# Kernel optimization log

Measured on AMD Instinct MI355X. Metric: run time of the kernel, lower is better.

## Reference

```python
import jax, jax.numpy as jnp
import numpy as np

ALPHA = 0.01  # alpha = input_scale * weight_scale (dequant scale)
BETA = 1.0    # bias scale, fixed to 1.0 in forward


def setup_inputs() -> dict:
    key = jax.random.key(0)
    k1, k2, k3 = jax.random.split(key, 3)
    # int8 values carried in int32 containers (schema has no int8 dtype)
    x = jax.random.randint(k1, (2, 2048, 4096), -127, 128, dtype=jnp.int32)
    weight = jax.random.randint(k2, (11008, 4096), -127, 128, dtype=jnp.int32)
    bias = jax.random.normal(k3, (1, 11008), dtype=jnp.float32)
    return {"x": x, "weight": weight, "bias": bias}


def reference(x, weight, bias):
    # x: [..., K] int8 activations, weight: [N, K] int8, bias: [1, N] fp32
    x_shape = x.shape
    x2 = x.reshape(-1, x_shape[-1]).astype(jnp.int8)   # [M, K]
    w8 = weight.astype(jnp.int8)                        # [N, K]
    acc = jnp.einsum('mk,nk->mn', x2, w8, preferred_element_type=jnp.int32)
    # fused dequant scale + fp32 bias add
    y = ALPHA * acc.astype(jnp.float32) + BETA * bias   # [M, N]
    return y.reshape(*x_shape[:-1], -1)
```

## Files before the change

kernel.cpp:

```cpp
#include <hip/hip_runtime.h>


#define M_DIM 4096
#define N_DIM 11008
#define K_DIM 4096
#define BM 256
#define BN 256
#define BK 128
#define NT (K_DIM / BK)
#define ALPHA 0.01f

typedef __attribute__((ext_vector_type(4))) int i32x4;

static __device__ __forceinline__ int pack4(int4 v) {
    return (v.x & 0xff) | ((v.y & 0xff) << 8) |
           ((v.z & 0xff) << 16) | ((unsigned)(v.w & 0xff) << 24);
}

__global__ __launch_bounds__(256) void pack_i8_kernel(
    const int4* __restrict__ x, int4* __restrict__ xout, int n16x,
    const int4* __restrict__ w, int4* __restrict__ wout, int n16_total)
{
    int i = blockIdx.x * blockDim.x + threadIdx.x;
    if (i >= n16_total) return;
    const int4* src;
    int4* dst;
    int idx;
    if (i < n16x) { src = x; dst = xout; idx = i; }
    else          { src = w; dst = wout; idx = i - n16x; }
    const int4* p = src + (size_t)4 * idx;
    int4 a = p[0], b = p[1], c = p[2], d = p[3];
    int4 r;
    r.x = pack4(a); r.y = pack4(b); r.z = pack4(c); r.w = pack4(d);
    dst[idx] = r;
}

#define GA0 (s_ + 8 * (s_ >> 3))
#define GA1 (8 + s_ + 8 * (s_ >> 3))
#define GB0 ((s_ & 3) + 8 * (s_ >> 2))
#define GB1 (4 + (s_ & 3) + 8 * (s_ >> 2))

#define STAGE(dstArr, srcB, T, GEXPR)                                          \
    _Pragma("unroll") for (int u_ = 0; u_ < 2; u_++) {                         \
        const int s_ = u_ * 8 + wave;                                          \
        const int G_ = (GEXPR);                                                \
        __builtin_amdgcn_global_load_lds(                                      \
            (const __attribute__((address_space(1))) void*)(                   \
                (srcB) + (size_t)(G_ * 8 + (lane >> 3)) * K_DIM +              \
                (size_t)(T) * BK + sch16),                                     \
            (__attribute__((address_space(3))) void*)((dstArr) + G_ * 1024 +   \
                                                      lane * 16),              \
            16, 0, 0);                                                         \
    }

#define READ_A(Arr, dst, IB)                                                   \
    _Pragma("unroll") for (int i_ = 0; i_ < 4; i_++)                           \
        _Pragma("unroll") for (int k_ = 0; k_ < 2; k_++)                       \
            dst[i_][k_] = *(const i32x4*)((Arr) + aoff[k_] + ((IB) + i_) * 2048);

#define READ_B(Arr, dst, JB)                                                   \
    _Pragma("unroll") for (int j_ = 0; j_ < 2; j_++)                           \
        _Pragma("unroll") for (int k_ = 0; k_ < 2; k_++)                       \
            dst[j_][k_] = *(const i32x4*)((Arr) + boff[k_] + ((JB) + j_) * 2048);

#define MFMA_G(af, bf, IB, JB)                                                 \
    __builtin_amdgcn_s_setprio(1);                                             \
    _Pragma("unroll") for (int i_ = 0; i_ < 4; i_++)                           \
        _Pragma("unroll") for (int j_ = 0; j_ < 2; j_++)                       \
            _Pragma("unroll") for (int k_ = 0; k_ < 2; k_++)                   \
                acc[(IB) + i_][(JB) + j_] =                                    \
                    __builtin_amdgcn_mfma_i32_16x16x64_i8(                     \
                        af[i_][k_], bf[j_][k_],                                \
                        acc[(IB) + i_][(JB) + j_], 0, 0, 0);                   \
    __builtin_amdgcn_s_setprio(0);

#define VMCNT_(N) asm volatile("s_waitcnt vmcnt(" #N ")" ::: "memory")
#define VMCNT(N) VMCNT_(N)
#define BAR() __builtin_amdgcn_s_barrier()

#define TILE(CA, CB, NA, NB, T, STG, V1, V2, V3, V4)                           \
    {                                                                          \
              \
        READ_A(CA, ra0, 0);                                                    \
        if (STG) { STAGE(NA, Abase, (T) + 1, GA0); }                           \
        VMCNT(V1);                                                             \
        BAR();                                                                 \
        READ_B(CB, rb01, 0);                                                   \
        MFMA_G(ra0, rb01, 0, 0);                                               \
        BAR();                                                                 \
                         \
        if (STG) { STAGE(NB, Bbase, (T) + 1, GB0); }                           \
        VMCNT(V2);                                                             \
        BAR();                                                                 \
        READ_B(CB, rb23, 2);                                                   \
        MFMA_G(ra0, rb23, 0, 2);                                               \
        BAR();                                                                 \
                          \
        if (STG) { STAGE(NB, Bbase, (T) + 1, GB1); }                           \
        VMCNT(V3);                                                             \
        BAR();                                                                 \
        READ_A(CA, ra1, 4);                                                    \
        MFMA_G(ra1, rb23, 4, 2);                                               \
        BAR();                                                                 \
                      \
        READ_B(CB, rb01, 0);                                                   \
        if (STG) { STAGE(NA, Abase, (T) + 1, GA1); }                           \
        VMCNT(V4);                                                             \
        BAR();                                                                 \
        MFMA_G(ra1, rb01, 4, 0);                                               \
        BAR();                                                                 \
    }

__global__ __launch_bounds__(512, 1) void gemm_i8_kernel(
    const char* __restrict__ A,
    const char* __restrict__ B,
    const float* __restrict__ bias,
    float* __restrict__ C)
{
    __shared__ __attribute__((aligned(16))) char As0[BM * BK];
    __shared__ __attribute__((aligned(16))) char Bs0[BN * BK];
    __shared__ __attribute__((aligned(16))) char As1[BM * BK];
    __shared__ __attribute__((aligned(16))) char Bs1[BN * BK];

    const int tid   = threadIdx.x;
    const int lane  = tid & 63;
    const int wave  = tid >> 6;
    const int waveM = (wave >> 2) * 128;
    const int waveN = (wave & 3) * 64;
    const int lrow  = lane & 15;
    const int lquad = lane >> 4;

    const int bid = blockIdx.x;
    const int xcd = bid & 7;
    const int loc = bid >> 3;
    const int bm  = (2 * xcd + (loc & 1)) * BM;
    const int bn  = (loc >> 1) * BN;

    const int sch16 = ((lane & 7) ^ ((lane >> 3) & 7)) << 4;
    const char* Abase = A + (size_t)bm * K_DIM;
    const char* Bbase = B + (size_t)bn * K_DIM;

    int aoff[2], boff[2];
#pragma unroll
    for (int ks = 0; ks < 2; ks++) {
        const int pos = ((ks * 4 + lquad) ^ (lrow & 7)) << 4;
        aoff[ks] = (waveM + lrow) * BK + pos;
        boff[ks] = (waveN + lrow) * BK + pos;
    }

    i32x4 acc[8][4] = {};
    i32x4 ra0[4][2], ra1[4][2], rb01[2][2], rb23[2][2];

    STAGE(As0, Abase, 0, GA0);
    STAGE(Bs0, Bbase, 0, GB0);
    STAGE(Bs0, Bbase, 0, GB1);
    STAGE(As0, Abase, 0, GA1);
    VMCNT(0);
    BAR();

#pragma unroll 1
    for (int t = 0; t < NT - 2; t += 2) {
        TILE(As0, Bs0, As1, Bs1, t,     1, 6, 6, 6, 6);
        TILE(As1, Bs1, As0, Bs0, t + 1, 1, 6, 6, 6, 6);
    }
    TILE(As0, Bs0, As1, Bs1, NT - 2, 1, 6, 6, 6, 6);
    TILE(As1, Bs1, As0, Bs0, NT - 1, 0, 4, 2, 0, 0);

#pragma unroll
    for (int i = 0; i < 8; i++) {
        const int r0 = bm + waveM + i * 16 + lquad * 4;
#pragma unroll
        for (int j = 0; j < 4; j++) {
            const int c0 = bn + waveN + j * 16 + lrow;
            const float bv = bias[c0];
#pragma unroll
            for (int r = 0; r < 4; r++) {
                C[(size_t)(r0 + r) * N_DIM + c0] = ALPHA * (float)acc[i][j][r] + bv;
            }
        }
    }
}

extern "C" void kernel_launch(void* const* d_in, const int* in_sizes, int n_in,
                              void* d_out, int out_size, void* d_ws, size_t ws_size,
                              hipStream_t stream) {
    const int*   x    = (const int*)d_in[0];
    const int*   w    = (const int*)d_in[1];
    const float* bias = (const float*)d_in[2];
    float*       out  = (float*)d_out;

    char* Ap = (char*)d_ws;
    char* Wp = (char*)d_ws + (size_t)M_DIM * K_DIM;

    const int n16x = M_DIM * K_DIM / 16;
    const int n16w = N_DIM * K_DIM / 16;
    const int n16  = n16x + n16w;
    pack_i8_kernel<<<n16 / 256, 256, 0, stream>>>(
        (const int4*)x, (int4*)Ap, n16x, (const int4*)w, (int4*)Wp, n16);

    gemm_i8_kernel<<<dim3((M_DIM / BM) * (N_DIM / BN)), 512, 0, stream>>>(
        Ap, Wp, bias, out);
}
```

Baseline: 541.6 us.

## Load B fragments directly from global into registers, bypassing LDS

Removes the LDS staging buffers for the weight (B) tile. Each wave now loads its B fragments straight from global memory into registers, one K-tile ahead, and the barrier count per tile drops from eight to two. The aim is to halve LDS traffic and shared-memory footprint and to cut synchronisation. The cost is uncoalesced 16-byte-per-lane global loads for B with no reuse across waves, plus longer VMCNT waits and more register pressure from double-buffered B fragments.

After: 604.8 us. +11.7%, slower.

```diff
diff --git a/kernel.cpp b/kernel.cpp
--- a/kernel.cpp
+++ b/kernel.cpp
@@ -37,8 +37,6 @@
 
 #define GA0 (s_ + 8 * (s_ >> 3))
 #define GA1 (8 + s_ + 8 * (s_ >> 3))
-#define GB0 ((s_ & 3) + 8 * (s_ >> 2))
-#define GB1 (4 + (s_ & 3) + 8 * (s_ >> 2))
 
 #define STAGE(dstArr, srcB, T, GEXPR)                                          \
     _Pragma("unroll") for (int u_ = 0; u_ < 2; u_++) {                         \
@@ -58,16 +56,20 @@
         _Pragma("unroll") for (int k_ = 0; k_ < 2; k_++)                       \
             dst[i_][k_] = *(const i32x4*)((Arr) + aoff[k_] + ((IB) + i_) * 2048);
 
-#define READ_B(Arr, dst, JB)                                                   \
+#define BLOAD01(dst, IMM)                                                      \
     _Pragma("unroll") for (int j_ = 0; j_ < 2; j_++)                           \
         _Pragma("unroll") for (int k_ = 0; k_ < 2; k_++)                       \
-            dst[j_][k_] = *(const i32x4*)((Arr) + boff[k_] + ((JB) + j_) * 2048);
+            dst[j_][k_] = *(const i32x4*)(bptr[j_] + (IMM) + k_ * 64);
+#define BLOAD23(dst, IMM)                                                      \
+    _Pragma("unroll") for (int j_ = 0; j_ < 2; j_++)                           \
+        _Pragma("unroll") for (int k_ = 0; k_ < 2; k_++)                       \
+            dst[j_][k_] = *(const i32x4*)(bptr[2 + j_] + (IMM) + k_ * 64);
 
 #define MFMA_G(af, bf, IB, JB)                                                 \
     __builtin_amdgcn_s_setprio(1);                                             \
-    _Pragma("unroll") for (int i_ = 0; i_ < 4; i_++)                           \
-        _Pragma("unroll") for (int j_ = 0; j_ < 2; j_++)                       \
-            _Pragma("unroll") for (int k_ = 0; k_ < 2; k_++)                   \
+    _Pragma("unroll") for (int k_ = 0; k_ < 2; k_++)                           \
+        _Pragma("unroll") for (int i_ = 0; i_ < 4; i_++)                       \
+            _Pragma("unroll") for (int j_ = 0; j_ < 2; j_++)                   \
                 acc[(IB) + i_][(JB) + j_] =                                    \
                     __builtin_amdgcn_mfma_i32_16x16x64_i8(                     \
                         af[i_][k_], bf[j_][k_],                                \
@@ -77,38 +79,26 @@
 #define VMCNT_(N) asm volatile("s_waitcnt vmcnt(" #N ")" ::: "memory")
 #define VMCNT(N) VMCNT_(N)
 #define BAR() __builtin_amdgcn_s_barrier()
+#define SCHEDB() __builtin_amdgcn_sched_barrier(0)
 
-#define TILE(CA, CB, NA, NB, T, STG, V1, V2, V3, V4)                           \
+#define TILE(CA, NA, B01c, B01n, T, KOFF, STG, V2, V4)                         \
     {                                                                          \
-              \
-        READ_A(CA, ra0, 0);                                                    \
+        READ_A(CA, ra, 0);                                             \
         if (STG) { STAGE(NA, Abase, (T) + 1, GA0); }                           \
-        VMCNT(V1);                                                             \
-        BAR();                                                                 \
-        READ_B(CB, rb01, 0);                                                   \
-        MFMA_G(ra0, rb01, 0, 0);                                               \
-        BAR();                                                                 \
-                         \
-        if (STG) { STAGE(NB, Bbase, (T) + 1, GB0); }                           \
+        MFMA_G(ra, B01c, 0, 0);                                  \
+        MFMA_G(ra, rb23, 0, 2);                                  \
+        if (STG) { BLOAD01(B01n, (KOFF) + 128);                                \
+                   STAGE(NA, Abase, (T) + 1, GA1); }                           \
         VMCNT(V2);                                                             \
-        BAR();                                                                 \
-        READ_B(CB, rb23, 2);                                                   \
-        MFMA_G(ra0, rb23, 0, 2);                                               \
-        BAR();                                                                 \
-                          \
-        if (STG) { STAGE(NB, Bbase, (T) + 1, GB1); }                           \
-        VMCNT(V3);                                                             \
-        BAR();                                                                 \
-        READ_A(CA, ra1, 4);                                                    \
-        MFMA_G(ra1, rb23, 4, 2);                                               \
-        BAR();                                                                 \
-                      \
-        READ_B(CB, rb01, 0);                                                   \
-        if (STG) { STAGE(NA, Abase, (T) + 1, GA1); }                           \
+        SCHEDB();                                                              \
+        BAR();                                                    \
+        READ_A(CA, ra, 4);                                             \
+        MFMA_G(ra, rb23, 4, 2);                                  \
+        if (STG) { BLOAD23(rb23, (KOFF) + 128); }                              \
+        MFMA_G(ra, B01c, 4, 0);                                  \
         VMCNT(V4);                                                             \
-        BAR();                                                                 \
-        MFMA_G(ra1, rb01, 4, 0);                                               \
-        BAR();                                                                 \
+        SCHEDB();                                                              \
+        BAR();                                                    \
     }
 
 __global__ __launch_bounds__(512, 1) void gemm_i8_kernel(
@@ -118,9 +108,7 @@
     float* __restrict__ C)
 {
     __shared__ __attribute__((aligned(16))) char As0[BM * BK];
-    __shared__ __attribute__((aligned(16))) char Bs0[BN * BK];
     __shared__ __attribute__((aligned(16))) char As1[BM * BK];
-    __shared__ __attribute__((aligned(16))) char Bs1[BN * BK];
 
     const int tid   = threadIdx.x;
     const int lane  = tid & 63;
@@ -138,33 +126,40 @@
 
     const int sch16 = ((lane & 7) ^ ((lane >> 3) & 7)) << 4;
     const char* Abase = A + (size_t)bm * K_DIM;
-    const char* Bbase = B + (size_t)bn * K_DIM;
 
-    int aoff[2], boff[2];
+    int aoff[2];
 #pragma unroll
     for (int ks = 0; ks < 2; ks++) {
         const int pos = ((ks * 4 + lquad) ^ (lrow & 7)) << 4;
         aoff[ks] = (waveM + lrow) * BK + pos;
-        boff[ks] = (waveN + lrow) * BK + pos;
     }
 
+    const char* bptr[4];
+#pragma unroll
+    for (int j = 0; j < 4; j++)
+        bptr[j] = B + (size_t)(bn + waveN + j * 16 + lrow) * K_DIM + lquad * 16;
+
     i32x4 acc[8][4] = {};
-    i32x4 ra0[4][2], ra1[4][2], rb01[2][2], rb23[2][2];
+    i32x4 ra[4][2], rbA[2][2], rbB[2][2], rb23[2][2];
 
     STAGE(As0, Abase, 0, GA0);
-    STAGE(Bs0, Bbase, 0, GB0);
-    STAGE(Bs0, Bbase, 0, GB1);
     STAGE(As0, Abase, 0, GA1);
+    BLOAD01(rbA, 0);
+    BLOAD23(rb23, 0);
     VMCNT(0);
     BAR();
 
 #pragma unroll 1
-    for (int t = 0; t < NT - 2; t += 2) {
-        TILE(As0, Bs0, As1, Bs1, t,     1, 6, 6, 6, 6);
-        TILE(As1, Bs1, As0, Bs0, t + 1, 1, 6, 6, 6, 6);
+    for (int t = 0; t < NT - 4; t += 2) {
+        TILE(As0, As1, rbA, rbB, t,     0,   1, 12, 10);
+        TILE(As1, As0, rbB, rbA, t + 1, 128, 1, 12, 10);
+#pragma unroll
+        for (int j = 0; j < 4; j++) bptr[j] += 256;
     }
-    TILE(As0, Bs0, As1, Bs1, NT - 2, 1, 6, 6, 6, 6);
-    TILE(As1, Bs1, As0, Bs0, NT - 1, 0, 4, 2, 0, 0);
+    TILE(As0, As1, rbA, rbB, NT - 4, 0,   1, 12, 10);
+    TILE(As1, As0, rbB, rbA, NT - 3, 128, 1, 12, 10);
+    TILE(As0, As1, rbA, rbB, NT - 2, 256, 1, 12, 10);
+    TILE(As1, As0, rbB, rbA, NT - 1, 384, 0, 4, 0);
 
 #pragma unroll
     for (int i = 0; i < 8; i++) {
```
